# Performance work log

Measured on AMD Instinct MI355X. Metric: run time of the kernel, lower is better.

The kernel has to match this reference:

```python
import jax, jax.numpy as jnp
import numpy as np
import math

B, T, IN_DIM = 2, 2048, 512
D, NH, MULT, N_LAYER = 512, 8, 4, 3
N = D * MULT // NH  # per-head latent dim = 256
OUT_DIM = 512
THETA = 2 ** 16


def get_freqs(n):
    t = jnp.arange(n, dtype=jnp.float32)
    q = jnp.floor(t / 2.0) * 2.0  # quantize(q=2)
    return 1.0 / (THETA ** (q / n)) / (2.0 * math.pi)


def ln(x, eps=1e-5):
    mu = jnp.mean(x, axis=-1, keepdims=True)
    var = jnp.var(x, axis=-1, keepdims=True)
    return (x - mu) * jax.lax.rsqrt(var + eps)


def rope(phases, v):
    # phases: [T, N] broadcastable to v [B, nh, T, N]
    p = (phases % 1.0) * (2.0 * math.pi)
    pc, ps = jnp.cos(p), jnp.sin(p)
    # interleave rotate: out[..., 2i] = -v[..., 2i+1], out[..., 2i+1] = v[..., 2i]
    v_rot = jnp.stack((-v[..., 1::2], v[..., ::2]), axis=-1).reshape(v.shape)
    return v * pc + v_rot * ps


def setup_inputs() -> dict:
    key = jax.random.key(0)
    ks = jax.random.split(key, 8)
    std = 0.02
    return {
        "x": jax.random.normal(ks[0], (B, T, IN_DIM), dtype=jnp.float32),
        "w_in": jax.random.normal(ks[1], (IN_DIM, D), dtype=jnp.float32) * std,
        "b_in": jnp.zeros((D,), dtype=jnp.float32),
        "encoder": jax.random.normal(ks[2], (NH, D, N), dtype=jnp.float32) * std,
        "encoder_v": jax.random.normal(ks[3], (NH, D, N), dtype=jnp.float32) * std,
        "decoder": jax.random.normal(ks[4], (NH * N, D), dtype=jnp.float32) * std,
        "head_w": jax.random.normal(ks[5], (D, OUT_DIM), dtype=jnp.float32) * std,
        "head_b": jnp.zeros((OUT_DIM,), dtype=jnp.float32),
    }


def reference(x, w_in, b_in, encoder, encoder_v, decoder, head_w, head_b):
    freqs = get_freqs(N)  # [N]
    t_idx = jnp.arange(T, dtype=jnp.float32)
    phases = t_idx[:, None] * freqs[None, :]  # [T, N]
    # strict lower-triangular causal mask (tril diagonal=-1)
    mask = (jnp.arange(T)[:, None] > jnp.arange(T)[None, :])  # [T, T]
    dec = decoder.reshape(NH, N, D)

    xs = ln(x @ w_in + b_in)  # [B, T, D]
    for _ in range(N_LAYER):
        x_res = xs
        x_sparse = jax.nn.relu(jnp.einsum('btd,hdn->bhtn', xs, encoder))  # [B,nh,T,N]
        QR = rope(phases, x_sparse)
        scores = jnp.einsum('bhtn,bhsn->bhts', QR, QR)
        scores = jnp.where(mask, scores, 0.0)
        yKV = jnp.einsum('bhts,bsd->bhtd', scores, xs)  # V = x (head-broadcast)
        yKV = ln(yKV)
        y_sparse = jax.nn.relu(jnp.einsum('bhtd,hdn->bhtn', yKV, encoder_v))
        xy_sparse = x_sparse * y_sparse  # dropout p=0 -> identity
        yMLP = jnp.einsum('bhtn,hnd->btd', xy_sparse, dec)
        xs = ln(x_res + ln(yMLP))
    logits = xs @ head_w + head_b
    return logits
```

## Files before the change

### kernel.cpp

```cpp
#include <hip/hip_runtime.h>
#include <math.h>

constexpr int B_  = 2;
constexpr int T_  = 2048;
constexpr int D_  = 512;
constexpr int NH_ = 8;
constexpr int NL_ = 256;
constexpr int HN_ = NH_ * NL_;
constexpr int BT_ = B_ * T_;

typedef __bf16 v8bf __attribute__((ext_vector_type(8)));
typedef float  v4f  __attribute__((ext_vector_type(4)));
typedef unsigned short us8 __attribute__((ext_vector_type(8)));
typedef unsigned short us4 __attribute__((ext_vector_type(4)));

__device__ inline unsigned short f2b(float f) {
    union { float f; unsigned u; } v{f};
    unsigned r = v.u + 0x7FFF + ((v.u >> 16) & 1);
    return (unsigned short)(r >> 16);
}
__device__ inline float b2f(unsigned short u) {
    union { unsigned u; float f; } v{(unsigned)u << 16};
    return v.f;
}

__device__ __forceinline__ void g2l16(const void* g, void* l) {
    __builtin_amdgcn_global_load_lds(
        (const __attribute__((address_space(1))) void*)g,
        (__attribute__((address_space(3))) void*)l, 16, 0, 0);
}

#define TILE_IDS                                              \
    int tid = threadIdx.x;                                    \
    int lane = tid & 63, wid = tid >> 6;                      \
    int wm = (wid & 1) * 64, wn = (wid >> 1) * 64;            \
    int ln16 = lane & 15, q = lane >> 4;                      \
    int srl = lane >> 2, scl = (lane & 3) * 8;                \
    (void)wm; (void)wn;

#define T128_STAGE(Ab, lda, Bb, ldb, k0, buf)                 \
    _Pragma("unroll")                                         \
    for (int ci = 0; ci < 4; ++ci) {                          \
        int c = wid * 4 + ci;                                 \
        if (c < 8) {                                          \
            int r = c * 16 + srl;                             \
            g2l16(Ab + (long)r * lda + (k0) + scl,            \
                  (char*)As[buf] + c * 1024);                 \
        } else {                                              \
            int r = (c - 8) * 16 + srl;                       \
            g2l16(Bb + (long)r * ldb + (k0) + scl,            \
                  (char*)Bs[buf] + (c - 8) * 1024);           \
        }                                                     \
    }

#define TILE_MFMA(Asx, Bsx)                                   \
    {                                                         \
        v8bf af[4], bfr[4];                                   \
        _Pragma("unroll")                                     \
        for (int r = 0; r < 4; ++r)                           \
            af[r] = *(const v8bf*)&Asx[wm + r * 16 + ln16][q * 8]; \
        _Pragma("unroll")                                     \
        for (int c = 0; c < 4; ++c)                           \
            bfr[c] = *(const v8bf*)&Bsx[wn + c * 16 + ln16][q * 8]; \
        _Pragma("unroll")                                     \
        for (int r = 0; r < 4; ++r)                           \
            _Pragma("unroll")                                 \
            for (int c = 0; c < 4; ++c)                       \
                acc[r][c] = __builtin_amdgcn_mfma_f32_16x16x32_bf16( \
                    af[r], bfr[c], acc[r][c], 0, 0, 0);       \
    }

template <int KS, bool RELU, bool MUL, bool BF16OUT, bool LNA>
__global__ __launch_bounds__(256) void gemm128(
    const unsigned short* __restrict__ A, int lda, long sA,
    const unsigned short* __restrict__ Bt, int ldb, long sB,
    void* __restrict__ Cv, int ldc, long sC,
    const unsigned short* __restrict__ mulp, int K,
    const float* __restrict__ muinv, const float* __restrict__ colsum) {
    constexpr int NHF = KS / 32;
    int m0 = blockIdx.y * 128, n0 = blockIdx.x * 128, z = blockIdx.z;
    __shared__ unsigned short As[2][NHF][128][32];
    __shared__ unsigned short Bs[2][NHF][128][32];
    const unsigned short* Ab = A  + (long)z * sA + (long)m0 * lda;
    const unsigned short* Bb = Bt + (long)z * sB + (long)n0 * ldb;
    TILE_IDS
    v4f acc[4][4] = {};
    auto stageK = [&](int k0, int buf) {
        #pragma unroll
        for (int h = 0; h < NHF; ++h)
            #pragma unroll
            for (int ci = 0; ci < 4; ++ci) {
                int c = wid * 4 + ci;
                if (c < 8)
                    g2l16(Ab + (long)(c * 16 + srl) * lda + k0 + h * 32 + scl,
                          (char*)As[buf][h] + c * 1024);
                else
                    g2l16(Bb + (long)((c - 8) * 16 + srl) * ldb + k0 + h * 32 +
                              scl,
                          (char*)Bs[buf][h] + (c - 8) * 1024);
            }
    };
    stageK(0, 0);
    __syncthreads();
    int cur = 0;
    for (int k0 = 0; k0 < K; k0 += KS) {
        if (k0 + KS < K) stageK(k0 + KS, cur ^ 1);
        #pragma unroll
        for (int h = 0; h < NHF; ++h)
            TILE_MFMA(As[cur][h], Bs[cur][h])
        __syncthreads();
        cur ^= 1;
    }
    float* Cf = (float*)Cv;
    unsigned short* Cb = (unsigned short*)Cv;
    long zoff = (long)z * sC;
    #pragma unroll
    for (int r = 0; r < 4; ++r)
        #pragma unroll
        for (int c = 0; c < 4; ++c)
            #pragma unroll
            for (int e = 0; e < 4; ++e) {
                int row = m0 + wm + r * 16 + q * 4 + e;
                int col = n0 + wn + c * 16 + ln16;
                float v = acc[r][c][e];
                if (LNA) {
                    float2 mi = *(const float2*)&muinv[((long)z * BT_ + row) * 2];
                    float cs = colsum[(long)z * NL_ + col];
                    v = mi.y * (v - mi.x * cs);
                }
                if (RELU) v = fmaxf(v, 0.f);
                long idx = zoff + (long)row * ldc + col;
                if (MUL) v *= b2f(mulp[idx]);
                if (BF16OUT) Cb[idx] = f2b(v);
                else         Cf[idx] = v;
            }
}

__global__ __launch_bounds__(256) void enc_rope(
    const unsigned short* __restrict__ A,
    const unsigned short* __restrict__ Bt,
    unsigned short* __restrict__ xsp,
    unsigned short* __restrict__ qrh,
    unsigned short* __restrict__ qrT) {
    int m0 = blockIdx.y * 128, n0 = blockIdx.x * 128;
    __shared__ unsigned short As[4][128][32];
    __shared__ unsigned short Bs[4][128][32];
    unsigned short (*lt)[136] = (unsigned short(*)[136])&As[0][0][0];
    const unsigned short* Ab = A + (long)m0 * 512;
    const unsigned short* Bb = Bt + (long)n0 * 512;
    TILE_IDS
    v4f acc[4][4] = {};
    auto stage = [&](int t) {
        int k0 = t * 32, buf = t & 3;
        #pragma unroll
        for (int ci = 0; ci < 4; ++ci) {
            int c = wid * 4 + ci;
            if (c < 8)
                g2l16(Ab + (long)(c * 16 + srl) * 512 + k0 + scl,
                      (char*)As[buf] + c * 1024);
            else
                g2l16(Bb + (long)((c - 8) * 16 + srl) * 512 + k0 + scl,
                      (char*)Bs[buf] + (c - 8) * 1024);
        }
    };
    stage(0);
    stage(1);
#define ER_STEP(T, VM)                                          \
    asm volatile("s_waitcnt vmcnt(" VM ")" ::: "memory");       \
    __builtin_amdgcn_s_barrier();                               \
    asm volatile("" ::: "memory");                              \
    if ((T) + 2 < 16) stage((T) + 2);                           \
    TILE_MFMA(As[(T) & 3], Bs[(T) & 3])
    ER_STEP(0, "4")  ER_STEP(1, "4")  ER_STEP(2, "4")  ER_STEP(3, "4")
    ER_STEP(4, "4")  ER_STEP(5, "4")  ER_STEP(6, "4")  ER_STEP(7, "4")
    ER_STEP(8, "4")  ER_STEP(9, "4")  ER_STEP(10, "4") ER_STEP(11, "4")
    ER_STEP(12, "4") ER_STEP(13, "4") ER_STEP(14, "4") ER_STEP(15, "0")
#undef ER_STEP
    __syncthreads();
    int bb = m0 >> 11;
    int tbase = m0 & (T_ - 1);
    #pragma unroll
    for (int r = 0; r < 4; ++r)
        #pragma unroll
        for (int c = 0; c < 4; ++c)
            #pragma unroll
            for (int e = 0; e < 4; ++e) {
                int rl = wm + r * 16 + q * 4 + e;
                int col = n0 + wn + c * 16 + ln16;
                float v = fmaxf(acc[r][c][e], 0.f);
                xsp[(long)(m0 + rl) * HN_ + col] = f2b(v);
                int n = col & (NL_ - 1);
                int n2 = n >> 1;
                float fr = exp2f(-(float)n2 * 0.125f) *
                           (float)(1.0 / (2.0 * M_PI));
                float ph = (float)(tbase + rl) * fr;
                ph = (ph - floorf(ph)) * (float)(2.0 * M_PI);
                float s, cc;
                __sincosf(ph, &s, &cc);
                float vp = __shfl_xor(v, 1, 64);
                float o = (n & 1) ? (v * cc + vp * s) : (v * cc - vp * s);
                int hh = col >> 8;
                qrh[((long)(bb * 8 + hh) * T_ + tbase + rl) * NL_ + n] = f2b(o);
                lt[wn + c * 16 + ln16][rl] = f2b(o);
            }
    __syncthreads();
    {
        int nrow = tid >> 1, tseg = (tid & 1) * 64;
        int colg = n0 + nrow;
        int hh = colg >> 8, nn = colg & (NL_ - 1);
        long ob = ((long)(bb * 8 + hh) * NL_ + nn) * T_ + tbase + tseg;
        #pragma unroll
        for (int u = 0; u < 16; ++u)
            *(us4*)&qrT[ob + u * 4] = *(const us4*)&lt[nrow][tseg + u * 4];
    }
}

__global__ __launch_bounds__(256) void ct_gemm(
    const unsigned short* __restrict__ xsT,
    const unsigned short* __restrict__ qrT,
    unsigned short* __restrict__ Ct) {
    int z = blockIdx.x, nt = blockIdx.y;
    int j = blockIdx.z >> 2, mt = blockIdx.z & 3;
    int b = z >> 3;
    const unsigned short* Ab =
        xsT + (long)b * D_ * T_ + (long)(mt * 128) * T_ + j * 256;
    const unsigned short* Bb =
        qrT + (long)z * NL_ * T_ + (long)(nt * 128) * T_ + j * 256;
    __shared__ unsigned short As[2][128][32];
    __shared__ unsigned short Bs[2][128][32];
    TILE_IDS
    v4f acc[4][4] = {};
    T128_STAGE(Ab, T_, Bb, T_, 0, 0)
    __syncthreads();
    int cur = 0;
    for (int k0 = 0; k0 < 256; k0 += 32) {
        if (k0 + 32 < 256) { T128_STAGE(Ab, T_, Bb, T_, k0 + 32, cur ^ 1) }
        TILE_MFMA(As[cur], Bs[cur])
        __syncthreads();
        cur ^= 1;
    }
    unsigned short* ob = Ct + ((long)z * 8 + j) * 512 * 256;
    #pragma unroll
    for (int r = 0; r < 4; ++r)
        #pragma unroll
        for (int c = 0; c < 4; ++c)
            #pragma unroll
            for (int e = 0; e < 4; ++e) {
                int row = mt * 128 + wm + r * 16 + q * 4 + e;
                int col = nt * 128 + wn + c * 16 + ln16;
                ob[(long)row * 256 + col] = f2b(acc[r][c][e]);
            }
}

__global__ __launch_bounds__(256) void prefix_k(unsigned short* __restrict__ Ct) {
    int z = blockIdx.x, dg = blockIdx.y;
    int d = dg * 8 + (threadIdx.x >> 5);
    int n0 = (threadIdx.x & 31) * 8;
    long base = ((long)z * 8) * 512 * 256 + (long)d * 256 + n0;
    constexpr long S = 512 * 256;
    us8 vals[8];
    #pragma unroll
    for (int i = 0; i < 8; ++i)
        vals[i] = *(const us8*)&Ct[base + (long)i * S];
    float acc[8] = {};
    #pragma unroll
    for (int i = 0; i < 8; ++i) {
        us8 o;
        #pragma unroll
        for (int e = 0; e < 8; ++e) o[e] = f2b(acc[e]);
        *(us8*)&Ct[base + (long)i * S] = o;
        #pragma unroll
        for (int e = 0; e < 8; ++e) acc[e] += b2f(vals[i][e]);
    }
}

__global__ __launch_bounds__(256) void sdiag(const unsigned short* __restrict__ qr,
                                             unsigned short* __restrict__ Sd) {
    int z = blockIdx.x, i = blockIdx.y, qq = blockIdx.z;
    int qm = (qq + 1) >> 1, qn = qq >> 1;
    const unsigned short* Ab =
        qr + ((long)z * T_ + i * 256 + qm * 128) * NL_;
    const unsigned short* Bb =
        qr + ((long)z * T_ + i * 256 + qn * 128) * NL_;
    bool dual = (qm != qn);
    __shared__ unsigned short As[2][128][32];
    __shared__ unsigned short Bs[2][128][32];
    TILE_IDS
    v4f acc[4][4] = {};
    auto stg = [&](int k0, int buf) {
        #pragma unroll
        for (int ci = 0; ci < 2; ++ci) {
            int c = wid * 2 + ci;
            g2l16(Ab + (long)(c * 16 + srl) * NL_ + k0 + scl,
                  (char*)As[buf] + c * 1024);
            if (dual)
                g2l16(Bb + (long)(c * 16 + srl) * NL_ + k0 + scl,
                      (char*)Bs[buf] + c * 1024);
        }
    };
    stg(0, 0);
    __syncthreads();
    int cur = 0;
    for (int k0 = 0; k0 < NL_; k0 += 32) {
        if (k0 + 32 < NL_) stg(k0 + 32, cur ^ 1);
        if (dual) { TILE_MFMA(As[cur], Bs[cur]) }
        else      { TILE_MFMA(As[cur], As[cur]) }
        __syncthreads();
        cur ^= 1;
    }
    unsigned short* ob = Sd + ((long)z * 8 + i) * 65536;
    #pragma unroll
    for (int r = 0; r < 4; ++r)
        #pragma unroll
        for (int c = 0; c < 4; ++c)
            #pragma unroll
            for (int e = 0; e < 4; ++e) {
                int row = wm + r * 16 + q * 4 + e;
                int col = wn + c * 16 + ln16;
                float v = acc[r][c][e];
                if (!dual && row <= col) v = 0.f;
                ob[(qm * 128 + row) * 256 + qn * 128 + col] = f2b(v);
            }
}

__global__ __launch_bounds__(256) void pxg(
    const unsigned short* __restrict__ qr,
    const unsigned short* __restrict__ Pt,
    const unsigned short* __restrict__ Sd,
    const unsigned short* __restrict__ xsT,
    unsigned short* __restrict__ ykvu,
    float* __restrict__ part) {
    int z = blockIdx.x, i = blockIdx.y, nt = blockIdx.z;
    int b = z >> 3, h = z & 7;
    int n0 = nt * 128;
    int i256 = i >> 1, hf2 = i & 1;
    const unsigned short* A1 = qr + ((long)z * T_ + i * 128) * NL_;
    const unsigned short* B1 =
        Pt + ((long)z * 8 + i256) * 512 * 256 + (long)n0 * 256;
    const unsigned short* A2 = Sd + ((long)z * 8 + i256) * 65536 +
                               (long)hf2 * 128 * 256;
    const unsigned short* B2 =
        xsT + (long)b * D_ * T_ + (long)n0 * T_ + i256 * 256;
    __shared__ unsigned short As[2][128][32];
    __shared__ unsigned short Bs[2][128][32];
    __shared__ float sred[128][2][2];
    TILE_IDS
    v4f acc[4][4] = {};
    int NS = 12 + hf2 * 4;
    auto stage = [&](int s) {
        const unsigned short* Ap;
        const unsigned short* Bp;
        long lda, ldb;
        int k0;
        if (s < 8) { Ap = A1; lda = NL_; Bp = B1; ldb = 256; k0 = s * 32; }
        else       { Ap = A2; lda = 256; Bp = B2; ldb = T_;  k0 = (s - 8) * 32; }
        int bi = s & 1;
        #pragma unroll
        for (int ci = 0; ci < 4; ++ci) {
            int c = wid * 4 + ci;
            if (c < 8)
                g2l16(Ap + (long)(c * 16 + srl) * lda + k0 + scl,
                      (char*)As[bi] + c * 1024);
            else
                g2l16(Bp + (long)((c - 8) * 16 + srl) * ldb + k0 + scl,
                      (char*)Bs[bi] + (c - 8) * 1024);
        }
    };
    stage(0);
    __syncthreads();
    for (int s = 0; s < NS; ++s) {
        if (s + 1 < NS) stage(s + 1);
        int bi = s & 1;
        TILE_MFMA(As[bi], Bs[bi])
        __syncthreads();
    }
    long obase = ((long)h * BT_ + (long)b * T_ + i * 128) * D_ + n0;
    #pragma unroll
    for (int r = 0; r < 4; ++r) {
        float s1[4] = {}, s2[4] = {};
        #pragma unroll
        for (int c = 0; c < 4; ++c)
            #pragma unroll
            for (int e = 0; e < 4; ++e) {
                float v = acc[r][c][e];
                s1[e] += v;
                s2[e] += v * v;
                int rl = wm + r * 16 + q * 4 + e;
                int col = wn + c * 16 + ln16;
                ykvu[obase + (long)rl * D_ + col] = f2b(v);
            }
        #pragma unroll
        for (int e = 0; e < 4; ++e) {
            #pragma unroll
            for (int off = 1; off < 16; off <<= 1) {
                s1[e] += __shfl_xor(s1[e], off, 64);
                s2[e] += __shfl_xor(s2[e], off, 64);
            }
            if (ln16 == 0) {
                int rl = wm + r * 16 + q * 4 + e;
                sred[rl][wid >> 1][0] = s1[e];
                sred[rl][wid >> 1][1] = s2[e];
            }
        }
    }
    __syncthreads();
    if (tid < 128) {
        float a = sred[tid][0][0] + sred[tid][1][0];
        float sq = sred[tid][0][1] + sred[tid][1][1];
        long pb = ((((long)z * 16 + i) * 4 + nt) * 128 + tid) * 2;
        part[pb] = a;
        part[pb + 1] = sq;
    }
}

__global__ __launch_bounds__(128) void lnstats(const float* __restrict__ part,
                                               float* __restrict__ muinv) {
    int z = blockIdx.x, i = blockIdx.y, t = threadIdx.x;
    long pb = ((((long)z * 16 + i) * 4) * 128 + t) * 2;
    float s1 = part[pb] + part[pb + 256] + part[pb + 512] + part[pb + 768];
    float s2 = part[pb + 1] + part[pb + 257] + part[pb + 513] + part[pb + 769];
    float mu = s1 * (1.0f / 512.0f);
    float var = s2 * (1.0f / 512.0f) - mu * mu;
    float inv = rsqrtf(var + 1e-5f);
    int b = z >> 3, h = z & 7;
    long row = (long)h * BT_ + (long)b * T_ + i * 128 + t;
    muinv[row * 2]     = mu;
    muinv[row * 2 + 1] = inv;
}

__global__ __launch_bounds__(256) void colsum_k(
    const unsigned short* __restrict__ encvT, float* __restrict__ cs) {
    int lane = threadIdx.x & 63, wv = threadIdx.x >> 6;
    int g = blockIdx.x * 4 + wv;
    us8 v = *(const us8*)&encvT[(long)g * 512 + lane * 8];
    float s = 0.f;
    #pragma unroll
    for (int e = 0; e < 8; ++e) s += b2f(v[e]);
    #pragma unroll
    for (int off = 1; off < 64; off <<= 1) s += __shfl_xor(s, off, 64);
    if (lane == 0) cs[g] = s;
}

__global__ __launch_bounds__(256) void trans_cast(
    const float* __restrict__ in, long sIn, unsigned short* __restrict__ out,
    long sOut, int R, int Cc) {
    __shared__ float tl[32][33];
    int z = blockIdx.z;
    int r0 = blockIdx.y * 32, c0 = blockIdx.x * 32;
    int tx = threadIdx.x & 31, ty = threadIdx.x >> 5;
    const float* ip = in + (long)z * sIn;
    unsigned short* op = out + (long)z * sOut;
    #pragma unroll
    for (int j = 0; j < 4; ++j)
        tl[ty + j * 8][tx] = ip[(long)(r0 + ty + j * 8) * Cc + c0 + tx];
    __syncthreads();
    #pragma unroll
    for (int j = 0; j < 4; ++j)
        op[(long)(c0 + ty + j * 8) * R + r0 + tx] = f2b(tl[tx][ty + j * 8]);
}

__global__ __launch_bounds__(256) void trans16(
    const unsigned short* __restrict__ in, long sIn,
    unsigned short* __restrict__ out, long sOut, int R, int Cc) {
    __shared__ unsigned short tl[32][34];
    int z = blockIdx.z;
    int r0 = blockIdx.y * 32, c0 = blockIdx.x * 32;
    int tx = threadIdx.x & 31, ty = threadIdx.x >> 5;
    const unsigned short* ip = in + (long)z * sIn;
    unsigned short* op = out + (long)z * sOut;
    #pragma unroll
    for (int j = 0; j < 4; ++j)
        tl[ty + j * 8][tx] = ip[(long)(r0 + ty + j * 8) * Cc + c0 + tx];
    __syncthreads();
    #pragma unroll
    for (int j = 0; j < 4; ++j)
        op[(long)(c0 + ty + j * 8) * R + r0 + tx] = tl[tx][ty + j * 8];
}

__global__ __launch_bounds__(256) void cast_b(const float* __restrict__ in,
                                              unsigned short* __restrict__ out) {
    long i = ((long)blockIdx.x * 256 + threadIdx.x) * 4;
    float4 v = *(const float4*)&in[i];
    ushort4 o;
    o.x = f2b(v.x); o.y = f2b(v.y); o.z = f2b(v.z); o.w = f2b(v.w);
    *(ushort4*)&out[i] = o;
}

__global__ __launch_bounds__(256) void add_out4(const float* __restrict__ t,
                                                long slice,
                                                const float* __restrict__ bias,
                                                float* __restrict__ o) {
    long i = ((long)blockIdx.x * 256 + threadIdx.x) * 4;
    float4 v0 = *(const float4*)&t[i];
    float4 v1 = *(const float4*)&t[i + slice];
    float4 v2 = *(const float4*)&t[i + 2 * slice];
    float4 v3 = *(const float4*)&t[i + 3 * slice];
    float4 bv = *(const float4*)&bias[i & 511];
    float4 r;
    r.x = v0.x + v1.x + v2.x + v3.x + bv.x;
    r.y = v0.y + v1.y + v2.y + v3.y + bv.y;
    r.z = v0.z + v1.z + v2.z + v3.z + bv.z;
    r.w = v0.w + v1.w + v2.w + v3.w + bv.w;
    *(float4*)&o[i] = r;
}

__device__ inline float2 block_reduce2(float a, float b) {
    __shared__ float sa[4], sb[4];
    #pragma unroll
    for (int off = 32; off; off >>= 1) {
        a += __shfl_down(a, off, 64);
        b += __shfl_down(b, off, 64);
    }
    __syncthreads();
    int w = threadIdx.x >> 6;
    if ((threadIdx.x & 63) == 0) { sa[w] = a; sb[w] = b; }
    __syncthreads();
    return make_float2(sa[0] + sa[1] + sa[2] + sa[3],
                       sb[0] + sb[1] + sb[2] + sb[3]);
}
__device__ inline float2 ln_pair(float2 v) {
    float2 s = block_reduce2(v.x + v.y, 0.f);
    float mu = s.x * (1.0f / 512.0f);
    float dx = v.x - mu, dy = v.y - mu;
    float2 q = block_reduce2(dx * dx + dy * dy, 0.f);
    float inv = rsqrtf(q.x * (1.0f / 512.0f) + 1e-5f);
    return make_float2(dx * inv, dy * inv);
}

__global__ __launch_bounds__(256) void ln_dual4(const float* __restrict__ t,
                                                long slice,
                                                const float* __restrict__ bias,
                                                float* __restrict__ outf,
                                                unsigned short* __restrict__ outb) {
    long row = blockIdx.x;
    int c = threadIdx.x * 2;
    long i = row * 512 + c;
    float2 v0 = *(const float2*)&t[i];
    float2 v1 = *(const float2*)&t[i + slice];
    float2 v2 = *(const float2*)&t[i + 2 * slice];
    float2 v3 = *(const float2*)&t[i + 3 * slice];
    float2 bv = *(const float2*)&bias[c];
    float2 v = make_float2(v0.x + v1.x + v2.x + v3.x + bv.x,
                           v0.y + v1.y + v2.y + v3.y + bv.y);
    float2 o = ln_pair(v);
    *(float2*)&outf[i] = o;
    ushort2 ob; ob.x = f2b(o.x); ob.y = f2b(o.y);
    *(ushort2*)&outb[i] = ob;
}

__global__ __launch_bounds__(256) void combine_dual4(
    const float* __restrict__ t, long slice, const float* __restrict__ xres,
    float* __restrict__ outf, unsigned short* __restrict__ outb) {
    long row = blockIdx.x;
    int c = threadIdx.x * 2;
    long i = row * 512 + c;
    float2 v0 = *(const float2*)&t[i];
    float2 v1 = *(const float2*)&t[i + slice];
    float2 v2 = *(const float2*)&t[i + 2 * slice];
    float2 v3 = *(const float2*)&t[i + 3 * slice];
    float2 y = make_float2(v0.x + v1.x + v2.x + v3.x,
                           v0.y + v1.y + v2.y + v3.y);
    float2 l = ln_pair(y);
    float2 r = *(const float2*)&xres[i];
    float2 z = make_float2(r.x + l.x, r.y + l.y);
    float2 o = ln_pair(z);
    *(float2*)&outf[i] = o;
    ushort2 ob; ob.x = f2b(o.x); ob.y = f2b(o.y);
    *(ushort2*)&outb[i] = ob;
}

extern "C" void kernel_launch(void* const* d_in, const int* in_sizes, int n_in,
                              void* d_out, int out_size, void* d_ws,
                              size_t ws_size, hipStream_t stream) {
    const float* x      = (const float*)d_in[0];
    const float* w_in   = (const float*)d_in[1];
    const float* b_in   = (const float*)d_in[2];
    const float* enc    = (const float*)d_in[3];
    const float* enc_v  = (const float*)d_in[4];
    const float* dec    = (const float*)d_in[5];
    const float* head_w = (const float*)d_in[6];
    const float* head_b = (const float*)d_in[7];
    float* out = (float*)d_out;

    char* w = (char*)d_ws;
    auto alloc = [&](size_t bytes) { void* p = (void*)w; w += bytes; return p; };
    unsigned short* w_inT = (unsigned short*)alloc((size_t)512 * 512 * 2);
    unsigned short* headT = (unsigned short*)alloc((size_t)512 * 512 * 2);
    unsigned short* encT  = (unsigned short*)alloc((size_t)NH_ * NL_ * D_ * 2);
    unsigned short* encvT = (unsigned short*)alloc((size_t)NH_ * NL_ * D_ * 2);
    unsigned short* decT  = (unsigned short*)alloc((size_t)D_ * HN_ * 2);
    unsigned short* xb    = (unsigned short*)alloc((size_t)BT_ * D_ * 2);
    float*          tmp   = (float*)alloc((size_t)4 * BT_ * D_ * 4);
    float*          xsf0  = (float*)alloc((size_t)BT_ * D_ * 4);
    float*          xsf1  = (float*)alloc((size_t)BT_ * D_ * 4);
    unsigned short* xs_b  = (unsigned short*)alloc((size_t)BT_ * D_ * 2);
    unsigned short* xsT   = (unsigned short*)alloc((size_t)B_ * D_ * T_ * 2);
    unsigned short* xsp   = (unsigned short*)alloc((size_t)BT_ * HN_ * 2);
    unsigned short* qrh   = (unsigned short*)alloc((size_t)BT_ * HN_ * 2);
    unsigned short* qrT   = (unsigned short*)alloc((size_t)BT_ * HN_ * 2);
    unsigned short* Ct    = (unsigned short*)alloc((size_t)128 * 512 * 256 * 2);
    unsigned short* Sd    = (unsigned short*)alloc((size_t)128 * 256 * 256 * 2);
    unsigned short* ykv   = (unsigned short*)alloc((size_t)NH_ * BT_ * D_ * 2);
    float*          part  = (float*)alloc((size_t)256 * 4 * 128 * 2 * 4);
    float*          muinv = (float*)alloc((size_t)NH_ * BT_ * 2 * 4);
    float*          csum  = (float*)alloc((size_t)HN_ * 4);
    const long SL = (long)BT_ * D_;

    cast_b<<<BT_ * D_ / 1024, 256, 0, stream>>>(x, xb);
    trans_cast<<<dim3(16, 16, 1), 256, 0, stream>>>(w_in, 0, w_inT, 0, 512, 512);
    trans_cast<<<dim3(16, 16, 1), 256, 0, stream>>>(head_w, 0, headT, 0, 512, 512);
    trans_cast<<<dim3(8, 16, 8), 256, 0, stream>>>(enc, (long)D_ * NL_, encT,
                                                   (long)NL_ * D_, D_, NL_);
    trans_cast<<<dim3(8, 16, 8), 256, 0, stream>>>(enc_v, (long)D_ * NL_, encvT,
                                                   (long)NL_ * D_, D_, NL_);
    trans_cast<<<dim3(16, 64, 1), 256, 0, stream>>>(dec, 0, decT, 0, HN_, D_);
    colsum_k<<<HN_ / 4, 256, 0, stream>>>(encvT, csum);

    gemm128<64, false, false, false, false>
        <<<dim3(4, 32, 4), 256, 0, stream>>>(xb, D_, 128, w_inT, D_, 128, tmp,
                                             D_, SL, nullptr, 128, nullptr,
                                             nullptr);
    ln_dual4<<<BT_, 256, 0, stream>>>(tmp, SL, b_in, xsf0, xs_b);
    trans16<<<dim3(16, 64, 2), 256, 0, stream>>>(xs_b, (long)T_ * D_, xsT,
                                                 (long)D_ * T_, T_, D_);

    float* xin = xsf0;
    float* xout = xsf1;
    for (int l = 0; l < 3; ++l) {
        enc_rope<<<dim3(16, 32), 256, 0, stream>>>(xs_b, encT, xsp, qrh, qrT);
        ct_gemm<<<dim3(16, 2, 32), 256, 0, stream>>>(xsT, qrT, Ct);
        prefix_k<<<dim3(16, 64), 256, 0, stream>>>(Ct);
        sdiag<<<dim3(16, 8, 3), 256, 0, stream>>>(qrh, Sd);
        pxg<<<dim3(16, 16, 4), 256, 0, stream>>>(qrh, Ct, Sd, xsT, ykv, part);
        lnstats<<<dim3(16, 16), 128, 0, stream>>>(part, muinv);
        gemm128<64, true, true, true, true>
            <<<dim3(2, 32, 8), 256, 0, stream>>>(
                ykv, D_, (long)BT_ * D_, encvT, D_, (long)NL_ * D_, xsp, HN_,
                NL_, xsp, 512, muinv, csum);
        gemm128<64, false, false, false, false>
            <<<dim3(4, 32, 4), 256, 0, stream>>>(
                xsp, HN_, 512, decT, HN_, 512, tmp, D_, SL, nullptr, 512,
                nullptr, nullptr);
        combine_dual4<<<BT_, 256, 0, stream>>>(tmp, SL, xin, xout, xs_b);
        trans16<<<dim3(16, 64, 2), 256, 0, stream>>>(xs_b, (long)T_ * D_, xsT,
                                                     (long)D_ * T_, T_, D_);
        float* t = xin; xin = xout; xout = t;
    }

    gemm128<64, false, false, false, false>
        <<<dim3(4, 32, 4), 256, 0, stream>>>(xs_b, D_, 128, headT, D_, 128, tmp,
                                             D_, SL, nullptr, 128, nullptr,
                                             nullptr);
    add_out4<<<BT_ * 512 / 1024, 256, 0, stream>>>(tmp, SL, head_b, out);
}
```

Before: 581.8 us.

## Switch GEMM kernels to triple-buffered LDS pipeline with vmcnt waits

Replaces the double-buffered, full-syncthreads K loops in gemm128, ct_gemm, sdiag and pxg with a three-stage ring buffer. Loads are issued two stages ahead, and each step waits with s_waitcnt vmcnt plus a bare s_barrier, so one stage of global-to-LDS loads stays in flight during the MFMAs. The aim is to hide global load latency and cut the number of full barriers per K step. In exchange, gemm128 moves from 64-wide K stages to 32-wide ones, and LDS use grows in the kernels that were double-buffered at 32.

```diff
diff --git a/kernel.cpp b/kernel.cpp
--- a/kernel.cpp
+++ b/kernel.cpp
@@ -30,6 +30,13 @@
         (__attribute__((address_space(3))) void*)l, 16, 0, 0);
 }
 
+#define VMCNT4 asm volatile("s_waitcnt vmcnt(4)" ::: "memory")
+#define VMCNT2 asm volatile("s_waitcnt vmcnt(2)" ::: "memory")
+#define VMCNT0 asm volatile("s_waitcnt vmcnt(0)" ::: "memory")
+#define BARRIER_FENCE                                   \
+    __builtin_amdgcn_s_barrier();                       \
+    asm volatile("" ::: "memory")
+
 #define TILE_IDS                                              \
     int tid = threadIdx.x;                                    \
     int lane = tid & 63, wid = tid >> 6;                      \
@@ -37,21 +44,6 @@
     int ln16 = lane & 15, q = lane >> 4;                      \
     int srl = lane >> 2, scl = (lane & 3) * 8;                \
     (void)wm; (void)wn;
-
-#define T128_STAGE(Ab, lda, Bb, ldb, k0, buf)                 \
-    _Pragma("unroll")                                         \
-    for (int ci = 0; ci < 4; ++ci) {                          \
-        int c = wid * 4 + ci;                                 \
-        if (c < 8) {                                          \
-            int r = c * 16 + srl;                             \
-            g2l16(Ab + (long)r * lda + (k0) + scl,            \
-                  (char*)As[buf] + c * 1024);                 \
-        } else {                                              \
-            int r = (c - 8) * 16 + srl;                       \
-            g2l16(Bb + (long)r * ldb + (k0) + scl,            \
-                  (char*)Bs[buf] + (c - 8) * 1024);           \
-        }                                                     \
-    }
 
 #define TILE_MFMA(Asx, Bsx)                                   \
     {                                                         \
@@ -70,46 +62,44 @@
                     af[r], bfr[c], acc[r][c], 0, 0, 0);       \
     }
 
-template <int KS, bool RELU, bool MUL, bool BF16OUT, bool LNA>
+template <bool RELU, bool MUL, bool BF16OUT, bool LNA>
 __global__ __launch_bounds__(256) void gemm128(
     const unsigned short* __restrict__ A, int lda, long sA,
     const unsigned short* __restrict__ Bt, int ldb, long sB,
     void* __restrict__ Cv, int ldc, long sC,
     const unsigned short* __restrict__ mulp, int K,
     const float* __restrict__ muinv, const float* __restrict__ colsum) {
-    constexpr int NHF = KS / 32;
     int m0 = blockIdx.y * 128, n0 = blockIdx.x * 128, z = blockIdx.z;
-    __shared__ unsigned short As[2][NHF][128][32];
-    __shared__ unsigned short Bs[2][NHF][128][32];
+    __shared__ unsigned short As[3][128][32];
+    __shared__ unsigned short Bs[3][128][32];
     const unsigned short* Ab = A  + (long)z * sA + (long)m0 * lda;
     const unsigned short* Bb = Bt + (long)z * sB + (long)n0 * ldb;
     TILE_IDS
     v4f acc[4][4] = {};
-    auto stageK = [&](int k0, int buf) {
-        #pragma unroll
-        for (int h = 0; h < NHF; ++h)
-            #pragma unroll
-            for (int ci = 0; ci < 4; ++ci) {
-                int c = wid * 4 + ci;
-                if (c < 8)
-                    g2l16(Ab + (long)(c * 16 + srl) * lda + k0 + h * 32 + scl,
-                          (char*)As[buf][h] + c * 1024);
-                else
-                    g2l16(Bb + (long)((c - 8) * 16 + srl) * ldb + k0 + h * 32 +
-                              scl,
-                          (char*)Bs[buf][h] + (c - 8) * 1024);
-            }
+    int NT = K >> 5;
+    auto stage = [&](int t, int buf) {
+        int k0 = t * 32;
+        #pragma unroll
+        for (int ci = 0; ci < 4; ++ci) {
+            int c = wid * 4 + ci;
+            if (c < 8)
+                g2l16(Ab + (long)(c * 16 + srl) * lda + k0 + scl,
+                      (char*)As[buf] + c * 1024);
+            else
+                g2l16(Bb + (long)((c - 8) * 16 + srl) * ldb + k0 + scl,
+                      (char*)Bs[buf] + (c - 8) * 1024);
+        }
     };
-    stageK(0, 0);
-    __syncthreads();
-    int cur = 0;
-    for (int k0 = 0; k0 < K; k0 += KS) {
-        if (k0 + KS < K) stageK(k0 + KS, cur ^ 1);
-        #pragma unroll
-        for (int h = 0; h < NHF; ++h)
-            TILE_MFMA(As[cur][h], Bs[cur][h])
-        __syncthreads();
-        cur ^= 1;
+    stage(0, 0);
+    if (NT > 1) stage(1, 1);
+    int bcur = 0, bnxt = 2;
+    for (int t = 0; t < NT; ++t) {
+        if (t + 1 < NT) { VMCNT4; } else { VMCNT0; }
+        BARRIER_FENCE;
+        if (t + 2 < NT) stage(t + 2, bnxt);
+        TILE_MFMA(As[bcur], Bs[bcur])
+        bcur = bcur + 1 == 3 ? 0 : bcur + 1;
+        bnxt = bnxt + 1 == 3 ? 0 : bnxt + 1;
     }
     float* Cf = (float*)Cv;
     unsigned short* Cb = (unsigned short*)Cv;
@@ -165,16 +155,17 @@
     };
     stage(0);
     stage(1);
-#define ER_STEP(T, VM)                                          \
-    asm volatile("s_waitcnt vmcnt(" VM ")" ::: "memory");       \
-    __builtin_amdgcn_s_barrier();                               \
-    asm volatile("" ::: "memory");                              \
+#define ER_STEP(T, W)                                           \
+    W;                                                          \
+    BARRIER_FENCE;                                              \
     if ((T) + 2 < 16) stage((T) + 2);                           \
     TILE_MFMA(As[(T) & 3], Bs[(T) & 3])
-    ER_STEP(0, "4")  ER_STEP(1, "4")  ER_STEP(2, "4")  ER_STEP(3, "4")
-    ER_STEP(4, "4")  ER_STEP(5, "4")  ER_STEP(6, "4")  ER_STEP(7, "4")
-    ER_STEP(8, "4")  ER_STEP(9, "4")  ER_STEP(10, "4") ER_STEP(11, "4")
-    ER_STEP(12, "4") ER_STEP(13, "4") ER_STEP(14, "4") ER_STEP(15, "0")
+    ER_STEP(0, VMCNT4)  ER_STEP(1, VMCNT4)  ER_STEP(2, VMCNT4)
+    ER_STEP(3, VMCNT4)  ER_STEP(4, VMCNT4)  ER_STEP(5, VMCNT4)
+    ER_STEP(6, VMCNT4)  ER_STEP(7, VMCNT4)  ER_STEP(8, VMCNT4)
+    ER_STEP(9, VMCNT4)  ER_STEP(10, VMCNT4) ER_STEP(11, VMCNT4)
+    ER_STEP(12, VMCNT4) ER_STEP(13, VMCNT4) ER_STEP(14, VMCNT4)
+    ER_STEP(15, VMCNT0)
 #undef ER_STEP
     __syncthreads();
     int bb = m0 >> 11;
@@ -226,18 +217,33 @@
         xsT + (long)b * D_ * T_ + (long)(mt * 128) * T_ + j * 256;
     const unsigned short* Bb =
         qrT + (long)z * NL_ * T_ + (long)(nt * 128) * T_ + j * 256;
-    __shared__ unsigned short As[2][128][32];
-    __shared__ unsigned short Bs[2][128][32];
+    __shared__ unsigned short As[3][128][32];
+    __shared__ unsigned short Bs[3][128][32];
     TILE_IDS
     v4f acc[4][4] = {};
-    T128_STAGE(Ab, T_, Bb, T_, 0, 0)
-    __syncthreads();
-    int cur = 0;
-    for (int k0 = 0; k0 < 256; k0 += 32) {
-        if (k0 + 32 < 256) { T128_STAGE(Ab, T_, Bb, T_, k0 + 32, cur ^ 1) }
-        TILE_MFMA(As[cur], Bs[cur])
-        __syncthreads();
-        cur ^= 1;
+    auto stage = [&](int t, int buf) {
+        int k0 = t * 32;
+        #pragma unroll
+        for (int ci = 0; ci < 4; ++ci) {
+            int c = wid * 4 + ci;
+            if (c < 8)
+                g2l16(Ab + (long)(c * 16 + srl) * T_ + k0 + scl,
+                      (char*)As[buf] + c * 1024);
+            else
+                g2l16(Bb + (long)((c - 8) * 16 + srl) * T_ + k0 + scl,
+                      (char*)Bs[buf] + (c - 8) * 1024);
+        }
+    };
+    stage(0, 0);
+    stage(1, 1);
+    int bcur = 0, bnxt = 2;
+    for (int t = 0; t < 8; ++t) {
+        if (t + 1 < 8) { VMCNT4; } else { VMCNT0; }
+        BARRIER_FENCE;
+        if (t + 2 < 8) stage(t + 2, bnxt);
+        TILE_MFMA(As[bcur], Bs[bcur])
+        bcur = bcur + 1 == 3 ? 0 : bcur + 1;
+        bnxt = bnxt + 1 == 3 ? 0 : bnxt + 1;
     }
     unsigned short* ob = Ct + ((long)z * 8 + j) * 512 * 256;
     #pragma unroll
@@ -283,11 +289,12 @@
     const unsigned short* Bb =
         qr + ((long)z * T_ + i * 256 + qn * 128) * NL_;
     bool dual = (qm != qn);
-    __shared__ unsigned short As[2][128][32];
-    __shared__ unsigned short Bs[2][128][32];
+    __shared__ unsigned short As[3][128][32];
+    __shared__ unsigned short Bs[3][128][32];
     TILE_IDS
     v4f acc[4][4] = {};
-    auto stg = [&](int k0, int buf) {
+    auto stage = [&](int t, int buf) {
+        int k0 = t * 32;
         #pragma unroll
         for (int ci = 0; ci < 2; ++ci) {
             int c = wid * 2 + ci;
@@ -298,15 +305,18 @@
                       (char*)Bs[buf] + c * 1024);
         }
     };
-    stg(0, 0);
-    __syncthreads();
-    int cur = 0;
-    for (int k0 = 0; k0 < NL_; k0 += 32) {
-        if (k0 + 32 < NL_) stg(k0 + 32, cur ^ 1);
-        if (dual) { TILE_MFMA(As[cur], Bs[cur]) }
-        else      { TILE_MFMA(As[cur], As[cur]) }
-        __syncthreads();
-        cur ^= 1;
+    stage(0, 0);
+    stage(1, 1);
+    int bcur = 0, bnxt = 2;
+    for (int t = 0; t < 8; ++t) {
+        if (t + 1 < 8) { if (dual) { VMCNT4; } else { VMCNT2; } }
+        else           { VMCNT0; }
+        BARRIER_FENCE;
+        if (t + 2 < 8) stage(t + 2, bnxt);
+        if (dual) { TILE_MFMA(As[bcur], Bs[bcur]) }
+        else      { TILE_MFMA(As[bcur], As[bcur]) }
+        bcur = bcur + 1 == 3 ? 0 : bcur + 1;
+        bnxt = bnxt + 1 == 3 ? 0 : bnxt + 1;
     }
     unsigned short* ob = Sd + ((long)z * 8 + i) * 65536;
     #pragma unroll
@@ -341,38 +351,40 @@
                                (long)hf2 * 128 * 256;
     const unsigned short* B2 =
         xsT + (long)b * D_ * T_ + (long)n0 * T_ + i256 * 256;
-    __shared__ unsigned short As[2][128][32];
-    __shared__ unsigned short Bs[2][128][32];
+    __shared__ unsigned short As[3][128][32];
+    __shared__ unsigned short Bs[3][128][32];
     __shared__ float sred[128][2][2];
     TILE_IDS
     v4f acc[4][4] = {};
     int NS = 12 + hf2 * 4;
-    auto stage = [&](int s) {
+    auto stage = [&](int s, int buf) {
         const unsigned short* Ap;
         const unsigned short* Bp;
         long lda, ldb;
         int k0;
         if (s < 8) { Ap = A1; lda = NL_; Bp = B1; ldb = 256; k0 = s * 32; }
         else       { Ap = A2; lda = 256; Bp = B2; ldb = T_;  k0 = (s - 8) * 32; }
-        int bi = s & 1;
         #pragma unroll
         for (int ci = 0; ci < 4; ++ci) {
             int c = wid * 4 + ci;
             if (c < 8)
                 g2l16(Ap + (long)(c * 16 + srl) * lda + k0 + scl,
-                      (char*)As[bi] + c * 1024);
+                      (char*)As[buf] + c * 1024);
             else
                 g2l16(Bp + (long)((c - 8) * 16 + srl) * ldb + k0 + scl,
-                      (char*)Bs[bi] + (c - 8) * 1024);
+                      (char*)Bs[buf] + (c - 8) * 1024);
         }
     };
-    stage(0);
-    __syncthreads();
+    stage(0, 0);
+    stage(1, 1);
+    int bcur = 0, bnxt = 2;
     for (int s = 0; s < NS; ++s) {
-        if (s + 1 < NS) stage(s + 1);
-        int bi = s & 1;
-        TILE_MFMA(As[bi], Bs[bi])
-        __syncthreads();
+        if (s + 1 < NS) { VMCNT4; } else { VMCNT0; }
+        BARRIER_FENCE;
+        if (s + 2 < NS) stage(s + 2, bnxt);
+        TILE_MFMA(As[bcur], Bs[bcur])
+        bcur = bcur + 1 == 3 ? 0 : bcur + 1;
+        bnxt = bnxt + 1 == 3 ? 0 : bnxt + 1;
     }
     long obase = ((long)h * BT_ + (long)b * T_ + i * 128) * D_ + n0;
     #pragma unroll
@@ -616,7 +628,7 @@
     trans_cast<<<dim3(16, 64, 1), 256, 0, stream>>>(dec, 0, decT, 0, HN_, D_);
     colsum_k<<<HN_ / 4, 256, 0, stream>>>(encvT, csum);
 
-    gemm128<64, false, false, false, false>
+    gemm128<false, false, false, false>
         <<<dim3(4, 32, 4), 256, 0, stream>>>(xb, D_, 128, w_inT, D_, 128, tmp,
                                              D_, SL, nullptr, 128, nullptr,
                                              nullptr);
@@ -633,11 +645,11 @@
         sdiag<<<dim3(16, 8, 3), 256, 0, stream>>>(qrh, Sd);
         pxg<<<dim3(16, 16, 4), 256, 0, stream>>>(qrh, Ct, Sd, xsT, ykv, part);
         lnstats<<<dim3(16, 16), 128, 0, stream>>>(part, muinv);
-        gemm128<64, true, true, true, true>
+        gemm128<true, true, true, true>
             <<<dim3(2, 32, 8), 256, 0, stream>>>(
                 ykv, D_, (long)BT_ * D_, encvT, D_, (long)NL_ * D_, xsp, HN_,
                 NL_, xsp, 512, muinv, csum);
-        gemm128<64, false, false, false, false>
+        gemm128<false, false, false, false>
             <<<dim3(4, 32, 4), 256, 0, stream>>>(
                 xsp, HN_, 512, decT, HN_, 512, tmp, D_, SL, nullptr, 512,
                 nullptr, nullptr);
@@ -647,7 +659,7 @@
         float* t = xin; xin = xout; xout = t;
     }
 
-    gemm128<64, false, false, false, false>
+    gemm128<false, false, false, false>
         <<<dim3(4, 32, 4), 256, 0, stream>>>(xs_b, D_, 128, headT, D_, 128, tmp,
                                              D_, SL, nullptr, 128, nullptr,
                                              nullptr);
```

Measured after the change: 645.4 us. +10.9%, slower.
